# Kernel optimization log

Hardware: AMD Instinct MI355X
Metric: run time of the kernel (lower is better)

The kernel has to match this reference:

```python
import jax, jax.numpy as jnp
import numpy as np

BN_EPS = 1e-3  # keras BatchNormalization default epsilon
B, T, D, V = 2048, 100, 64, 200000
N_OTHER, V_OTHER, D_OTHER = 2, 10000, 32
DNN = (256, 128, 64)


def _gru(seq_x, Wx, Wh, b, valid, att=None):
    """GRU / AUGRU scan. seq_x [B,T,D]; valid [B,T] bool; att [B,T] or None.
    AUGRU: update gate z is scaled by the attention score a_t;
    invalid (padded) steps hold the previous state (dynamic length)."""
    Bs, Ts, _ = seq_x.shape
    H = Wh.shape[0]
    xproj = jnp.einsum('btd,dh->bth', seq_x, Wx) + b          # [B,T,3H]
    xproj = jnp.transpose(xproj, (1, 0, 2))                    # [T,B,3H]
    v = jnp.transpose(valid, (1, 0))[:, :, None]               # [T,B,1]
    if att is None:
        a = jnp.ones((Ts, Bs, 1), seq_x.dtype)
    else:
        a = jnp.transpose(att, (1, 0))[:, :, None]
    h0 = jnp.zeros((Bs, H), seq_x.dtype)

    def step(h, inp):
        xp, vi, ai = inp
        xz, xr, xh = jnp.split(xp, 3, -1)
        hz, hr, hh = jnp.split(h @ Wh, 3, -1)
        z = jax.nn.sigmoid(xz + hz) * ai
        r = jax.nn.sigmoid(xr + hr)
        cand = jnp.tanh(xh + r * hh)
        hn = (1.0 - z) * h + z * cand
        hn = jnp.where(vi, hn, h)
        return hn, hn

    final, seq = jax.lax.scan(step, h0, (xproj, v, a))
    return final, jnp.transpose(seq, (1, 0, 2))                # [B,T,H]


def _dice(x, alpha):
    # Dice activation, inference-mode BN (moving mean 0, var 1)
    p = jax.nn.sigmoid(x * (1.0 / np.sqrt(1.0 + BN_EPS)))
    return p * x + (1.0 - p) * alpha * x


def _attention(q, keys, mask, W1, b1, W2, b2, W3, b3):
    # DIN-style attention: MLP over [q, k, q-k, q*k], masked softmax over time
    qe = jnp.broadcast_to(q[:, None, :], keys.shape)
    info = jnp.concatenate([qe, keys, qe - keys, qe * keys], -1)   # [B,T,4D]
    h = jax.nn.sigmoid(info @ W1 + b1)
    h = jax.nn.sigmoid(h @ W2 + b2)
    logits = (h @ W3 + b3)[..., 0]                                  # [B,T]
    logits = jnp.where(mask, logits, jnp.float32(-1e9))
    return jax.nn.softmax(logits, axis=-1)


def setup_inputs() -> dict:
    key = jax.random.key(0)
    ks = jax.random.split(key, 32)
    s = 0.05
    inp = {
        'dense_inputs': jax.random.normal(ks[0], (B, 8), jnp.float32),
        'sparse_inputs': jax.random.randint(ks[1], (B, N_OTHER), 0, V_OTHER, jnp.int32),
        'seq_inputs': jax.random.randint(ks[2], (B, T, 1), 0, V, jnp.int32),
        'no_click_seq': jax.random.randint(ks[3], (B, T, 1), 0, V, jnp.int32),
        'item_inputs': jax.random.randint(ks[4], (B, 1), 0, V, jnp.int32),
        'hist_real_len': jax.random.randint(ks[5], (B,), 1, T + 1, jnp.int32),
        'emb_item': jax.random.normal(ks[6], (V, D), jnp.float32) * s,
        'emb_neg': jax.random.normal(ks[7], (V, D), jnp.float32) * s,
        'emb_other': jax.random.normal(ks[8], (N_OTHER, V_OTHER, D_OTHER), jnp.float32) * s,
        'gru1_Wx': jax.random.normal(ks[9], (D, 3 * D), jnp.float32) * s,
        'gru1_Wh': jax.random.normal(ks[10], (D, 3 * D), jnp.float32) * s,
        'gru1_b': jnp.zeros((3 * D,), jnp.float32),
        'att_W1': jax.random.normal(ks[11], (4 * D, 64), jnp.float32) * s,
        'att_b1': jnp.zeros((64,), jnp.float32),
        'att_W2': jax.random.normal(ks[12], (64, 16), jnp.float32) * s,
        'att_b2': jnp.zeros((16,), jnp.float32),
        'att_W3': jax.random.normal(ks[13], (16, 1), jnp.float32) * s,
        'att_b3': jnp.zeros((1,), jnp.float32),
        'gru2_Wx': jax.random.normal(ks[14], (D, 3 * D), jnp.float32) * s,
        'gru2_Wh': jax.random.normal(ks[15], (D, 3 * D), jnp.float32) * s,
        'gru2_b': jnp.zeros((3 * D,), jnp.float32),
    }
    in_dim = D + D + 8 + N_OTHER * D_OTHER  # final_state + target + other_info
    inp['bn_gamma'] = jnp.ones((in_dim,), jnp.float32)
    inp['bn_beta'] = jnp.zeros((in_dim,), jnp.float32)
    dims = (in_dim,) + DNN
    for i in range(3):
        inp[f'ffn_W{i}'] = jax.random.normal(ks[16 + i], (dims[i], dims[i + 1]), jnp.float32) * s
        inp[f'ffn_b{i}'] = jnp.zeros((dims[i + 1],), jnp.float32)
        inp[f'dice_a{i}'] = jnp.full((dims[i + 1],), 0.25, jnp.float32)
    inp['out_W'] = jax.random.normal(ks[20], (DNN[-1], 1), jnp.float32) * s
    inp['out_b'] = jnp.zeros((1,), jnp.float32)
    return inp


def reference(dense_inputs, sparse_inputs, seq_inputs, no_click_seq, item_inputs,
              hist_real_len, emb_item, emb_neg, emb_other, gru1_Wx, gru1_Wh, gru1_b,
              att_W1, att_b1, att_W2, att_b2, att_W3, att_b3, gru2_Wx, gru2_Wh, gru2_b,
              bn_gamma, bn_beta, ffn_W0, ffn_b0, dice_a0, ffn_W1, ffn_b1, dice_a1,
              ffn_W2, ffn_b2, dice_a2, out_W, out_b):
    # other (non-behavior) info: dense feats ++ other sparse embeddings
    other = jnp.concatenate(
        [dense_inputs] + [emb_other[i][sparse_inputs[:, i]] for i in range(N_OTHER)], -1)
    seq_embed = emb_item[seq_inputs[:, :, 0]]          # [B,T,D]
    neg_embed = emb_neg[no_click_seq[:, :, 0]]         # [B,T,D]
    target = emb_item[item_inputs[:, 0]]               # [B,D]
    mask = seq_inputs[:, :, 0] != 0                    # [B,T]
    valid = jnp.arange(T)[None, :] < hist_real_len[:, None]

    # interest extraction: plain GRU over behavior sequence
    _, seq_h = _gru(seq_embed, gru1_Wx, gru1_Wh, gru1_b, valid)

    # auxiliary loss: h_t should predict the next clicked item vs a negative
    m = mask[:, 1:].astype(seq_h.dtype)
    h = seq_h[:, :-1]
    p_pos = jax.nn.sigmoid(jnp.sum(h * seq_embed[:, 1:], -1))
    p_neg = jax.nn.sigmoid(jnp.sum(h * neg_embed[:, 1:], -1))
    aux_loss = -jnp.sum(m * (jnp.log(p_pos + 1e-8) + jnp.log(1.0 - p_neg + 1e-8))) / (jnp.sum(m) + 1e-8)

    # interest evolution: attention-gated AUGRU
    scores = _attention(target, seq_h, mask, att_W1, att_b1, att_W2, att_b2, att_W3, att_b3)
    final_state, _ = _gru(seq_h, gru2_Wx, gru2_Wh, gru2_b, valid, att=scores)

    x = jnp.concatenate([final_state, target, other], -1)
    x = bn_gamma * x * (1.0 / np.sqrt(1.0 + BN_EPS)) + bn_beta   # inference BN
    x = _dice(x @ ffn_W0 + ffn_b0, dice_a0)
    x = _dice(x @ ffn_W1 + ffn_b1, dice_a1)
    x = _dice(x @ ffn_W2 + ffn_b2, dice_a2)
    out = jax.nn.sigmoid(x @ out_W + out_b)                       # [B,1]
    return out, aux_loss
```

## Files before the change

kernel.cpp:

```cpp
#include <hip/hip_runtime.h>
#include <math.h>


#define DEV __device__ __forceinline__

constexpr int BB = 2048;
constexpr int TT = 100;

typedef __attribute__((ext_vector_type(8))) short bf16x8;
typedef __attribute__((ext_vector_type(4))) float f32x4;

#define MFMA16(a, b, c) __builtin_amdgcn_mfma_f32_16x16x32_bf16(a, b, c, 0, 0, 0)

DEV float sigmoidf_(float x) { return 1.0f / (1.0f + __expf(-x)); }
DEV float tanhf_(float x)    { return 1.0f - 2.0f / (__expf(2.0f * x) + 1.0f); }
DEV short f2bf(float f) {
    unsigned u = __float_as_uint(f);
    u = (u + 0x7FFFu + ((u >> 16) & 1u)) >> 16;
    return (short)u;
}
DEV float bf2f(short s) { return __uint_as_float(((unsigned)(unsigned short)s) << 16); }

__global__ void k_prep(const float* __restrict__ W1, float* Wq, float* Wk, float* Wp, float* aux_acc) {
    int i = blockIdx.x * 256 + threadIdx.x;
    if (i < 4096) {
        int k = i >> 6, c = i & 63;
        float a  = W1[k * 64 + c];
        float bb = W1[(64 + k) * 64 + c];
        float cc = W1[(128 + k) * 64 + c];
        float dd = W1[(192 + k) * 64 + c];
        Wq[i] = a + cc;
        Wk[i] = bb - cc;
        Wp[i] = dd;
    }
    if (blockIdx.x == 0 && threadIdx.x == 0) { aux_acc[0] = 0.0f; aux_acc[1] = 0.0f; }
}

__global__ __launch_bounds__(256)
void k_prepW(const float* __restrict__ Wa, const float* __restrict__ Wb,
             const float* __restrict__ Wc, const float* __restrict__ Wd,
             short* __restrict__ oa, short* __restrict__ ob,
             short* __restrict__ oc, short* __restrict__ od) {
    const float* W; short* o;
    switch (blockIdx.y) {
        case 0:  W = Wa; o = oa; break;
        case 1:  W = Wb; o = ob; break;
        case 2:  W = Wc; o = oc; break;
        default: W = Wd; o = od; break;
    }
    int d = blockIdx.x * 256 + threadIdx.x;
    int frag = d >> 9, l = (d >> 3) & 63, i = d & 7;
    int n = frag >> 1, kt = frag & 1;
    int k = kt * 32 + ((l >> 4) << 3) + i;
    int c = (n << 4) + (l & 15);
    o[d] = f2bf(W[k * 192 + c]);
}

__global__ __launch_bounds__(256)
void k_prepA(const float* __restrict__ Wk, const float* __restrict__ Wp,
             short* __restrict__ oK, short* __restrict__ oP) {
    int d = blockIdx.x * 256 + threadIdx.x;
    int mat = d >> 12, i = d & 4095;
    int f = i >> 9, l = (i >> 3) & 63, e = i & 7;
    int kt = f >> 2, n = f & 3;
    int k = kt * 32 + ((l >> 4) << 3) + e;
    int c = (n << 4) + (l & 15);
    if (mat == 0) oK[i] = f2bf(Wk[k * 64 + c]);
    else          oP[i] = f2bf(Wp[k * 64 + c]);
}

__global__ __launch_bounds__(64)
void k_target(const int* __restrict__ item, const float* __restrict__ emb_item,
              const float* __restrict__ Wq, const float* __restrict__ b1,
              float* target, float* qproj) {
    int b = blockIdx.x, c = threadIdx.x;
    __shared__ float q[64];
    int idx = item[b];
    float tv = emb_item[(size_t)idx * 64 + c];
    target[b * 64 + c] = tv;
    q[c] = tv;
    __syncthreads();
    float acc = b1[c];
#pragma unroll
    for (int k = 0; k < 64; ++k) acc = fmaf(q[k], Wq[k * 64 + c], acc);
    qproj[b * 64 + c] = acc;
}

template <int MODE>
__global__ __launch_bounds__(256, 1)
void k_scan(const int* __restrict__ seq_idx, const float* __restrict__ src,
            const short* __restrict__ WxB, const short* __restrict__ WhB,
            const float* __restrict__ bias, const int* __restrict__ hist_len,
            const float* __restrict__ scores,
            float* __restrict__ seq_out, float* __restrict__ final_out) {
    __shared__ short hA[2][1024];

    const int tid  = threadIdx.x;
    const int w    = tid >> 6;
    const int lane = tid & 63;
    const int lr   = lane & 15;
    const int kg   = lane >> 4;
    const int b0   = blockIdx.x * 8;

    for (int i = tid; i < 2048; i += 256) ((short*)hA)[i] = 0;

    bf16x8 bx[3][2], bh[3][2];
#pragma unroll
    for (int n3 = 0; n3 < 3; ++n3) {
        int n = w + n3 * 4;
#pragma unroll
        for (int kt = 0; kt < 2; ++kt) {
            bx[n3][kt] = *(const bf16x8*)(WxB + (((n * 2 + kt) * 64 + lane) << 3));
            bh[n3][kt] = *(const bf16x8*)(WhB + (((n * 2 + kt) * 64 + lane) << 3));
        }
    }

    const int   c0  = (w << 4) + lr;
    const float bz  = bias[c0];
    const float brr = bias[64 + c0];
    const float bhb = bias[128 + c0];
    const int   qc  = kg & 1;
    const bool  act = (kg < 2);

    int   hist[4];
    float h[4] = {0.f, 0.f, 0.f, 0.f};
#pragma unroll
    for (int j = 0; j < 4; ++j) hist[j] = hist_len[b0 + qc * 4 + j];

    const int rload = (lr < 8) ? lr : 7;
    float4 ec[4], en[4];
    float  scc[4] = {1.f, 1.f, 1.f, 1.f}, scn[4];

    {
        const float* eb;
        if (MODE == 0) { int idx = seq_idx[(b0 + rload) * TT]; eb = src + (size_t)idx * 64; }
        else           { eb = src + ((size_t)(b0 + rload) * TT) * 64; }
        ec[0] = *(const float4*)(eb + kg * 8);
        ec[1] = *(const float4*)(eb + kg * 8 + 4);
        ec[2] = *(const float4*)(eb + 32 + kg * 8);
        ec[3] = *(const float4*)(eb + 32 + kg * 8 + 4);
        if (MODE == 1) {
#pragma unroll
            for (int j = 0; j < 4; ++j) scc[j] = scores[(b0 + qc * 4 + j) * TT];
        }
    }
    __syncthreads();

    for (int t = 0; t < TT; ++t) {
        const int buf = t & 1;
        const int so0 = lr * 64 + (((kg    ) ^ (lr & 7)) << 3);
        const int so1 = lr * 64 + (((4 + kg) ^ (lr & 7)) << 3);
        bf16x8 ha0 = *(const bf16x8*)&hA[buf][so0];
        bf16x8 ha1 = *(const bf16x8*)&hA[buf][so1];

        if (t < TT - 1) {
            const float* eb;
            if (MODE == 0) { int idx = seq_idx[(b0 + rload) * TT + t + 1]; eb = src + (size_t)idx * 64; }
            else           { eb = src + ((size_t)(b0 + rload) * TT + (t + 1)) * 64; }
            en[0] = *(const float4*)(eb + kg * 8);
            en[1] = *(const float4*)(eb + kg * 8 + 4);
            en[2] = *(const float4*)(eb + 32 + kg * 8);
            en[3] = *(const float4*)(eb + 32 + kg * 8 + 4);
            if (MODE == 1) {
#pragma unroll
                for (int j = 0; j < 4; ++j) scn[j] = scores[(b0 + qc * 4 + j) * TT + t + 1];
            }
        }

        bf16x8 ea0, ea1;
        ea0[0] = f2bf(ec[0].x); ea0[1] = f2bf(ec[0].y); ea0[2] = f2bf(ec[0].z); ea0[3] = f2bf(ec[0].w);
        ea0[4] = f2bf(ec[1].x); ea0[5] = f2bf(ec[1].y); ea0[6] = f2bf(ec[1].z); ea0[7] = f2bf(ec[1].w);
        ea1[0] = f2bf(ec[2].x); ea1[1] = f2bf(ec[2].y); ea1[2] = f2bf(ec[2].z); ea1[3] = f2bf(ec[2].w);
        ea1[4] = f2bf(ec[3].x); ea1[5] = f2bf(ec[3].y); ea1[6] = f2bf(ec[3].z); ea1[7] = f2bf(ec[3].w);

        f32x4 az  = {0.f, 0.f, 0.f, 0.f};
        f32x4 ar  = {0.f, 0.f, 0.f, 0.f};
        f32x4 ahx = {0.f, 0.f, 0.f, 0.f};
        f32x4 ahh = {0.f, 0.f, 0.f, 0.f};
        az  = MFMA16(ea0, bx[0][0], az);  az  = MFMA16(ea1, bx[0][1], az);
        az  = MFMA16(ha0, bh[0][0], az);  az  = MFMA16(ha1, bh[0][1], az);
        ar  = MFMA16(ea0, bx[1][0], ar);  ar  = MFMA16(ea1, bx[1][1], ar);
        ar  = MFMA16(ha0, bh[1][0], ar);  ar  = MFMA16(ha1, bh[1][1], ar);
        ahx = MFMA16(ea0, bx[2][0], ahx); ahx = MFMA16(ea1, bx[2][1], ahx);
        ahh = MFMA16(ha0, bh[2][0], ahh); ahh = MFMA16(ha1, bh[2][1], ahh);

        if (act) {
#pragma unroll
            for (int j = 0; j < 4; ++j) {
                float a01  = (MODE == 1) ? scc[j] : 1.0f;
                float z    = sigmoidf_(az[j] + bz) * a01;
                float r    = sigmoidf_(ar[j] + brr);
                float cand = tanhf_(ahx[j] + bhb + r * ahh[j]);
                float hn   = h[j] + z * (cand - h[j]);
                h[j] = (t < hist[j]) ? hn : h[j];
                int rr = qc * 4 + j;
                int sw = rr * 64 + ((((c0 >> 3)) ^ (rr & 7)) << 3) + (c0 & 7);
                hA[buf ^ 1][sw] = f2bf(h[j]);
                if (MODE == 0)
                    seq_out[((size_t)(b0 + rr) * TT + t) * 64 + c0] = h[j];
            }
        }
        if (t < TT - 1) {
#pragma unroll
            for (int q4 = 0; q4 < 4; ++q4) ec[q4] = en[q4];
            if (MODE == 1) {
#pragma unroll
                for (int j = 0; j < 4; ++j) scc[j] = scn[j];
            }
        }
        __syncthreads();
    }

    if (MODE == 1 && act) {
#pragma unroll
        for (int j = 0; j < 4; ++j) {
            int rr = qc * 4 + j;
            final_out[(b0 + rr) * 64 + c0] = h[j];
        }
    }
}

__global__ __launch_bounds__(256)
void k_attn(const float* __restrict__ seq_h, const float* __restrict__ target,
            const float* __restrict__ qproj, const int* __restrict__ seq_idx,
            const short* __restrict__ WkB, const short* __restrict__ WpB,
            const float* __restrict__ W2g, const float* __restrict__ b2g,
            const float* __restrict__ W3g, const float* __restrict__ b3g,
            float* __restrict__ scores) {
    __shared__ __align__(16) short keysb[7168];
    __shared__ __align__(16) short pkb[7168];
    __shared__ float W2_s[1024];
    __shared__ float q_s[64], qp_s[64];
    __shared__ float b2_s[16], W3_s[16];
    __shared__ float lg[112];

    const int b = blockIdx.x, tid = threadIdx.x;
    const int w = tid >> 6, lane = tid & 63;

    bf16x8 BK[2][4], BP[2][4];
#pragma unroll
    for (int kt = 0; kt < 2; ++kt)
#pragma unroll
        for (int n = 0; n < 4; ++n) {
            BK[kt][n] = *(const bf16x8*)(WkB + (((kt * 4 + n) * 64 + lane) << 3));
            BP[kt][n] = *(const bf16x8*)(WpB + (((kt * 4 + n) * 64 + lane) << 3));
        }
    if (tid < 64)  { q_s[tid] = target[b * 64 + tid]; qp_s[tid] = qproj[b * 64 + tid]; }
    if (tid >= 64 && tid < 80) { b2_s[tid - 64] = b2g[tid - 64]; W3_s[tid - 64] = W3g[tid - 64]; }
    for (int i = tid; i < 1024; i += 256) W2_s[i] = W2g[i];
    __syncthreads();

    for (int i4 = tid; i4 < 1792; i4 += 256) {
        int r = i4 >> 4, c4 = i4 & 15;
        short4 kv, pv;
        if (r < TT) {
            float4 f = *(const float4*)(seq_h + (size_t)b * (TT * 64) + r * 64 + c4 * 4);
            float q0 = q_s[c4 * 4], q1 = q_s[c4 * 4 + 1], q2 = q_s[c4 * 4 + 2], q3 = q_s[c4 * 4 + 3];
            kv = make_short4(f2bf(f.x), f2bf(f.y), f2bf(f.z), f2bf(f.w));
            pv = make_short4(f2bf(f.x * q0), f2bf(f.y * q1), f2bf(f.z * q2), f2bf(f.w * q3));
        } else {
            kv = make_short4(0, 0, 0, 0); pv = kv;
        }
        int off = r * 128 + ((c4 * 8) ^ ((r & 7) << 4));
        *(short4*)((char*)keysb + off) = kv;
        *(short4*)((char*)pkb + off)   = pv;
    }
    __syncthreads();

    for (int rt = w; rt < 7; rt += 4) {
        const int r0 = rt * 16;
        const int arow = r0 + (lane & 15);
        const int kb = lane >> 4;
        bf16x8 AK[2], AP[2];
#pragma unroll
        for (int kt = 0; kt < 2; ++kt) {
            int off = arow * 128 + (((kt * 64) + kb * 16) ^ ((arow & 7) << 4));
            AK[kt] = *(const bf16x8*)((const char*)keysb + off);
            AP[kt] = *(const bf16x8*)((const char*)pkb + off);
        }
        f32x4 C[4];
#pragma unroll
        for (int n = 0; n < 4; ++n) { C[n] = (f32x4){0.f, 0.f, 0.f, 0.f}; }
#pragma unroll
        for (int n = 0; n < 4; ++n) {
            C[n] = MFMA16(AK[0], BK[0][n], C[n]);
            C[n] = MFMA16(AK[1], BK[1][n], C[n]);
            C[n] = MFMA16(AP[0], BP[0][n], C[n]);
            C[n] = MFMA16(AP[1], BP[1][n], C[n]);
        }
#pragma unroll
        for (int n = 0; n < 4; ++n) {
            int col = n * 16 + (lane & 15);
            float qp = qp_s[col];
#pragma unroll
            for (int j = 0; j < 4; ++j) {
                int row = r0 + (lane >> 4) * 4 + j;
                float h1 = sigmoidf_(C[n][j] + qp);
                int off = row * 128 + ((col * 2) ^ ((row & 7) << 4));
                *(short*)((char*)pkb + off) = f2bf(h1);
            }
        }
    }
    __syncthreads();

    {
        int t = tid >> 1, half = tid & 1;
        if (t < TT) {
            int j0 = half * 8;
            float acc[8];
#pragma unroll
            for (int jj = 0; jj < 8; ++jj) acc[jj] = b2_s[j0 + jj];
#pragma unroll
            for (int ch = 0; ch < 8; ++ch) {
                int off = t * 128 + ((ch * 16) ^ ((t & 7) << 4));
                bf16x8 hv = *(const bf16x8*)((const char*)pkb + off);
#pragma unroll
                for (int e = 0; e < 8; ++e) {
                    float hf = bf2f(hv[e]);
                    int k = ch * 8 + e;
#pragma unroll
                    for (int jj = 0; jj < 8; ++jj)
                        acc[jj] = fmaf(hf, W2_s[k * 16 + j0 + jj], acc[jj]);
                }
            }
            float part = 0.f;
#pragma unroll
            for (int jj = 0; jj < 8; ++jj) part += sigmoidf_(acc[jj]) * W3_s[j0 + jj];
            part += __shfl_xor(part, 1);
            if (half == 0) {
                bool m = (seq_idx[b * TT + t] != 0);
                lg[t] = m ? (part + b3g[0]) : -1e9f;
            }
        }
    }
    __syncthreads();

    if (w == 0) {
        float a  = lg[lane];
        float bv = (lane + 64 < TT) ? lg[lane + 64] : -1e30f;
        float mx = fmaxf(a, bv);
#pragma unroll
        for (int s = 32; s; s >>= 1) mx = fmaxf(mx, __shfl_xor(mx, s));
        float ea = __expf(a - mx);
        float eb = (lane + 64 < TT) ? __expf(bv - mx) : 0.f;
        float sum = ea + eb;
#pragma unroll
        for (int s = 32; s; s >>= 1) sum += __shfl_xor(sum, s);
        float inv = 1.0f / sum;
        scores[b * TT + lane] = ea * inv;
        if (lane + 64 < TT) scores[b * TT + lane + 64] = eb * inv;
    }
}

__global__ __launch_bounds__(64)
void k_aux(const float* __restrict__ seq_h, const int* __restrict__ seq_idx,
           const int* __restrict__ neg_idx, const float* __restrict__ emb_item,
           const float* __restrict__ emb_neg, float* aux_acc) {
    int b = blockIdx.x, l = threadIdx.x;
    float num = 0.0f;
    float den = 0.0f;
    for (int t = 0; t < TT - 1; ++t) {
        int ip = seq_idx[b * TT + t + 1];
        int in_ = neg_idx[b * TT + t + 1];
        float h = seq_h[(size_t)b * (TT * 64) + t * 64 + l];
        float dp = h * emb_item[(size_t)ip * 64 + l];
        float dn = h * emb_neg[(size_t)in_ * 64 + l];
#pragma unroll
        for (int s = 32; s; s >>= 1) { dp += __shfl_xor(dp, s); dn += __shfl_xor(dn, s); }
        if (l == 0 && ip != 0) {
            float pp = sigmoidf_(dp), pn = sigmoidf_(dn);
            num += __logf(pp + 1e-8f) + __logf(1.0f - pn + 1e-8f);
            den += 1.0f;
        }
    }
    if (l == 0) {
        atomicAdd(&aux_acc[0], num);
        atomicAdd(&aux_acc[1], den);
    }
}

__global__ __launch_bounds__(256)
void k_mlp(const float* __restrict__ final_state, const float* __restrict__ target,
           const float* __restrict__ dense, const int* __restrict__ sparse,
           const float* __restrict__ emb_other,
           const float* __restrict__ bng, const float* __restrict__ bnb,
           const float* __restrict__ W0, const float* __restrict__ bb0, const float* __restrict__ al0,
           const float* __restrict__ W1, const float* __restrict__ bb1, const float* __restrict__ al1,
           const float* __restrict__ W2, const float* __restrict__ bb2, const float* __restrict__ al2,
           const float* __restrict__ Wo, const float* __restrict__ bo,
           const float* __restrict__ aux_acc, float* __restrict__ out) {
    const float inv1 = 0.9995003747f;
    int tid = threadIdx.x, b0 = blockIdx.x * 8;
    __shared__ float x_s[8][200], h1_s[8][256], h2_s[8][128], h3_s[8][64];

    for (int i = tid; i < 8 * 200; i += 256) {
        int r = i / 200, cc = i - r * 200, b = b0 + r;
        float v;
        if (cc < 64)       v = final_state[b * 64 + cc];
        else if (cc < 128) v = target[b * 64 + cc - 64];
        else if (cc < 136) v = dense[b * 8 + cc - 128];
        else if (cc < 168) v = emb_other[(size_t)sparse[b * 2 + 0] * 32 + (cc - 136)];
        else               v = emb_other[(size_t)10000 * 32 + (size_t)sparse[b * 2 + 1] * 32 + (cc - 168)];
        x_s[r][cc] = fmaf(bng[cc] * inv1, v, bnb[cc]);
    }
    __syncthreads();
    {
        int r = tid >> 5, cb = tid & 31;
        float acc[8];
#pragma unroll
        for (int j = 0; j < 8; ++j) acc[j] = bb0[cb + 32 * j];
        for (int k = 0; k < 200; ++k) {
            float xv = x_s[r][k];
#pragma unroll
            for (int j = 0; j < 8; ++j) acc[j] = fmaf(xv, W0[k * 256 + cb + 32 * j], acc[j]);
        }
#pragma unroll
        for (int j = 0; j < 8; ++j) {
            float y = acc[j];
            float p = sigmoidf_(y * inv1);
            h1_s[r][cb + 32 * j] = y * (p + (1.0f - p) * al0[cb + 32 * j]);
        }
    }
    __syncthreads();
    {
        int r = tid >> 5, cb = tid & 31;
        float acc[4];
#pragma unroll
        for (int j = 0; j < 4; ++j) acc[j] = bb1[cb + 32 * j];
        for (int k = 0; k < 256; ++k) {
            float xv = h1_s[r][k];
#pragma unroll
            for (int j = 0; j < 4; ++j) acc[j] = fmaf(xv, W1[k * 128 + cb + 32 * j], acc[j]);
        }
#pragma unroll
        for (int j = 0; j < 4; ++j) {
            float y = acc[j];
            float p = sigmoidf_(y * inv1);
            h2_s[r][cb + 32 * j] = y * (p + (1.0f - p) * al1[cb + 32 * j]);
        }
    }
    __syncthreads();
    {
        int r = tid >> 5, cb = tid & 31;
        float acc[2] = {bb2[cb], bb2[cb + 32]};
        for (int k = 0; k < 128; ++k) {
            float xv = h2_s[r][k];
            acc[0] = fmaf(xv, W2[k * 64 + cb], acc[0]);
            acc[1] = fmaf(xv, W2[k * 64 + cb + 32], acc[1]);
        }
#pragma unroll
        for (int j = 0; j < 2; ++j) {
            float y = acc[j];
            float p = sigmoidf_(y * inv1);
            h3_s[r][cb + 32 * j] = y * (p + (1.0f - p) * al2[cb + 32 * j]);
        }
    }
    __syncthreads();
    {
        int r = tid >> 5, l = tid & 31;
        float v = h3_s[r][l] * Wo[l] + h3_s[r][l + 32] * Wo[l + 32];
#pragma unroll
        for (int s = 16; s; s >>= 1) v += __shfl_xor(v, s, 32);
        if (l == 0) out[b0 + r] = sigmoidf_(v + bo[0]);
    }
    if (blockIdx.x == 0 && tid == 0) {
        out[BB] = -aux_acc[0] / (aux_acc[1] + 1e-8f);
    }
}

extern "C" void kernel_launch(void* const* d_in, const int* in_sizes, int n_in,
                              void* d_out, int out_size, void* d_ws, size_t ws_size,
                              hipStream_t stream) {
    (void)in_sizes; (void)n_in; (void)out_size; (void)ws_size;
    const float* dense    = (const float*)d_in[0];
    const int*   sparse   = (const int*)d_in[1];
    const int*   seq_in   = (const int*)d_in[2];
    const int*   neg_in   = (const int*)d_in[3];
    const int*   item_in  = (const int*)d_in[4];
    const int*   hist     = (const int*)d_in[5];
    const float* emb_item = (const float*)d_in[6];
    const float* emb_neg  = (const float*)d_in[7];
    const float* emb_oth  = (const float*)d_in[8];
    const float* g1Wx = (const float*)d_in[9];
    const float* g1Wh = (const float*)d_in[10];
    const float* g1b  = (const float*)d_in[11];
    const float* aW1  = (const float*)d_in[12];
    const float* ab1  = (const float*)d_in[13];
    const float* aW2  = (const float*)d_in[14];
    const float* ab2  = (const float*)d_in[15];
    const float* aW3  = (const float*)d_in[16];
    const float* ab3  = (const float*)d_in[17];
    const float* g2Wx = (const float*)d_in[18];
    const float* g2Wh = (const float*)d_in[19];
    const float* g2b  = (const float*)d_in[20];
    const float* bng  = (const float*)d_in[21];
    const float* bnb  = (const float*)d_in[22];
    const float* W0   = (const float*)d_in[23];
    const float* b0f  = (const float*)d_in[24];
    const float* a0f  = (const float*)d_in[25];
    const float* W1f  = (const float*)d_in[26];
    const float* b1f  = (const float*)d_in[27];
    const float* a1f  = (const float*)d_in[28];
    const float* W2f  = (const float*)d_in[29];
    const float* b2f  = (const float*)d_in[30];
    const float* a2f  = (const float*)d_in[31];
    const float* Wo   = (const float*)d_in[32];
    const float* bo   = (const float*)d_in[33];

    float* ws          = (float*)d_ws;
    float* seq_h       = ws;
    float* scoresW     = seq_h + 13107200;
    float* target      = scoresW + 204800;
    float* qproj       = target + 131072;
    float* final_state = qproj + 131072;
    float* Wq          = final_state + 131072;
    float* Wk          = Wq + 4096;
    float* Wp          = Wk + 4096;
    short* WxB1        = (short*)(Wp + 4096);
    short* WhB1        = WxB1 + 12288;
    short* WxB2        = WhB1 + 12288;
    short* WhB2        = WxB2 + 12288;
    short* WkB         = WhB2 + 12288;
    short* WpB         = WkB + 4096;
    float* aux_acc     = (float*)(WpB + 4096);

    k_prep<<<16, 256, 0, stream>>>(aW1, Wq, Wk, Wp, aux_acc);
    k_prepW<<<dim3(48, 4), 256, 0, stream>>>(g1Wx, g1Wh, g2Wx, g2Wh, WxB1, WhB1, WxB2, WhB2);
    k_prepA<<<32, 256, 0, stream>>>(Wk, Wp, WkB, WpB);
    k_target<<<BB, 64, 0, stream>>>(item_in, emb_item, Wq, ab1, target, qproj);
    k_scan<0><<<256, 256, 0, stream>>>(seq_in, emb_item, WxB1, WhB1, g1b, hist, nullptr, seq_h, nullptr);
    k_attn<<<BB, 256, 0, stream>>>(seq_h, target, qproj, seq_in, WkB, WpB, aW2, ab2, aW3, ab3, scoresW);
    k_scan<1><<<256, 256, 0, stream>>>(seq_in, seq_h, WxB2, WhB2, g2b, hist, scoresW, nullptr, final_state);
    k_aux<<<BB, 64, 0, stream>>>(seq_h, seq_in, neg_in, emb_item, emb_neg, aux_acc);
    k_mlp<<<256, 256, 0, stream>>>(final_state, target, dense, sparse, emb_oth, bng, bnb,
                                   W0, b0f, a0f, W1f, b1f, a1f, W2f, b2f, a2f, Wo, bo,
                                   aux_acc, (float*)d_out);
}
```

Baseline: 598.4 us.

## Store GRU hidden sequence as bf16 and halve per-block batch rows in scans

The first GRU's hidden-state sequence is now written as bf16 instead of fp32, halving its memory traffic for the attention, second-scan and aux kernels, which read it directly. Each scan block now handles 4 batch rows instead of 8, doubling the grid to 512 blocks with 2 blocks per CU for more parallelism on the latency-bound recurrence. The per-step block barrier is replaced by a lightweight LDS-only wait plus s_barrier, and the bf16 conversion of the next embedding is deferred until after the gate math. The aux kernel is spread over 4 waves per batch row. The cost is a lower-precision stored hidden state (the aux loss sees bf16 h) and half of each MFMA tile's rows doing wasted work.

```diff
diff --git a/kernel.cpp b/kernel.cpp
--- a/kernel.cpp
+++ b/kernel.cpp
@@ -20,6 +20,12 @@
     return (short)u;
 }
 DEV float bf2f(short s) { return __uint_as_float(((unsigned)(unsigned short)s) << 16); }
+
+DEV void sync_lds() {
+    __builtin_amdgcn_sched_barrier(0);
+    asm volatile("s_waitcnt lgkmcnt(0)\n\ts_barrier" ::: "memory");
+    __builtin_amdgcn_sched_barrier(0);
+}
 
 __global__ void k_prep(const float* __restrict__ W1, float* Wq, float* Wk, float* Wp, float* aux_acc) {
     int i = blockIdx.x * 256 + threadIdx.x;
@@ -87,12 +93,13 @@
 }
 
 template <int MODE>
-__global__ __launch_bounds__(256, 1)
-void k_scan(const int* __restrict__ seq_idx, const float* __restrict__ src,
+__global__ __launch_bounds__(256, 2)
+void k_scan(const int* __restrict__ seq_idx, const float* __restrict__ embf,
+            const short* __restrict__ seqb,
             const short* __restrict__ WxB, const short* __restrict__ WhB,
             const float* __restrict__ bias, const int* __restrict__ hist_len,
             const float* __restrict__ scores,
-            float* __restrict__ seq_out, float* __restrict__ final_out) {
+            short* __restrict__ seq_out, float* __restrict__ final_out) {
     __shared__ short hA[2][1024];
 
     const int tid  = threadIdx.x;
@@ -100,7 +107,7 @@
     const int lane = tid & 63;
     const int lr   = lane & 15;
     const int kg   = lane >> 4;
-    const int b0   = blockIdx.x * 8;
+    const int b0   = blockIdx.x * 4;
 
     for (int i = tid; i < 2048; i += 256) ((short*)hA)[i] = 0;
 
@@ -119,70 +126,80 @@
     const float bz  = bias[c0];
     const float brr = bias[64 + c0];
     const float bhb = bias[128 + c0];
-    const int   qc  = kg & 1;
-    const bool  act = (kg < 2);
+    const bool  act = (kg == 0);
 
     int   hist[4];
     float h[4] = {0.f, 0.f, 0.f, 0.f};
 #pragma unroll
-    for (int j = 0; j < 4; ++j) hist[j] = hist_len[b0 + qc * 4 + j];
-
-    const int rload = (lr < 8) ? lr : 7;
-    float4 ec[4], en[4];
-    float  scc[4] = {1.f, 1.f, 1.f, 1.f}, scn[4];
+    for (int j = 0; j < 4; ++j) hist[j] = hist_len[b0 + j];
+
+    const int rload = (lr < 4) ? lr : 3;
+    bf16x8 ecb0, ecb1;
+    float  scc[4] = {1.f, 1.f, 1.f, 1.f};
 
     {
-        const float* eb;
-        if (MODE == 0) { int idx = seq_idx[(b0 + rload) * TT]; eb = src + (size_t)idx * 64; }
-        else           { eb = src + ((size_t)(b0 + rload) * TT) * 64; }
-        ec[0] = *(const float4*)(eb + kg * 8);
-        ec[1] = *(const float4*)(eb + kg * 8 + 4);
-        ec[2] = *(const float4*)(eb + 32 + kg * 8);
-        ec[3] = *(const float4*)(eb + 32 + kg * 8 + 4);
+        if (MODE == 0) {
+            int idx = seq_idx[(b0 + rload) * TT];
+            const float* eb = embf + (size_t)idx * 64;
+            float4 f0 = *(const float4*)(eb + kg * 8);
+            float4 f1 = *(const float4*)(eb + kg * 8 + 4);
+            float4 f2 = *(const float4*)(eb + 32 + kg * 8);
+            float4 f3 = *(const float4*)(eb + 32 + kg * 8 + 4);
+            ecb0[0] = f2bf(f0.x); ecb0[1] = f2bf(f0.y); ecb0[2] = f2bf(f0.z); ecb0[3] = f2bf(f0.w);
+            ecb0[4] = f2bf(f1.x); ecb0[5] = f2bf(f1.y); ecb0[6] = f2bf(f1.z); ecb0[7] = f2bf(f1.w);
+            ecb1[0] = f2bf(f2.x); ecb1[1] = f2bf(f2.y); ecb1[2] = f2bf(f2.z); ecb1[3] = f2bf(f2.w);
+            ecb1[4] = f2bf(f3.x); ecb1[5] = f2bf(f3.y); ecb1[6] = f2bf(f3.z); ecb1[7] = f2bf(f3.w);
+        } else {
+            const short* eb = seqb + ((size_t)(b0 + rload) * TT) * 64;
+            ecb0 = *(const bf16x8*)(eb + kg * 8);
+            ecb1 = *(const bf16x8*)(eb + 32 + kg * 8);
+        }
         if (MODE == 1) {
 #pragma unroll
-            for (int j = 0; j < 4; ++j) scc[j] = scores[(b0 + qc * 4 + j) * TT];
-        }
-    }
-    __syncthreads();
+            for (int j = 0; j < 4; ++j) scc[j] = scores[(b0 + j) * TT];
+        }
+    }
+    __syncthreads();
+
+    const int so0 = lr * 64 + (((kg    ) ^ (lr & 7)) << 3);
+    const int so1 = lr * 64 + (((4 + kg) ^ (lr & 7)) << 3);
 
     for (int t = 0; t < TT; ++t) {
         const int buf = t & 1;
-        const int so0 = lr * 64 + (((kg    ) ^ (lr & 7)) << 3);
-        const int so1 = lr * 64 + (((4 + kg) ^ (lr & 7)) << 3);
         bf16x8 ha0 = *(const bf16x8*)&hA[buf][so0];
         bf16x8 ha1 = *(const bf16x8*)&hA[buf][so1];
 
-        if (t < TT - 1) {
-            const float* eb;
-            if (MODE == 0) { int idx = seq_idx[(b0 + rload) * TT + t + 1]; eb = src + (size_t)idx * 64; }
-            else           { eb = src + ((size_t)(b0 + rload) * TT + (t + 1)) * 64; }
-            en[0] = *(const float4*)(eb + kg * 8);
-            en[1] = *(const float4*)(eb + kg * 8 + 4);
-            en[2] = *(const float4*)(eb + 32 + kg * 8);
-            en[3] = *(const float4*)(eb + 32 + kg * 8 + 4);
-            if (MODE == 1) {
-#pragma unroll
-                for (int j = 0; j < 4; ++j) scn[j] = scores[(b0 + qc * 4 + j) * TT + t + 1];
+        float4 f0, f1, f2, f3;
+        bf16x8 nb0, nb1;
+        float scn[4];
+        const bool haven = (t < TT - 1);
+        if (haven) {
+            if (MODE == 0) {
+                int idx = seq_idx[(b0 + rload) * TT + t + 1];
+                const float* eb = embf + (size_t)idx * 64;
+                f0 = *(const float4*)(eb + kg * 8);
+                f1 = *(const float4*)(eb + kg * 8 + 4);
+                f2 = *(const float4*)(eb + 32 + kg * 8);
+                f3 = *(const float4*)(eb + 32 + kg * 8 + 4);
+            } else {
+                const short* eb = seqb + ((size_t)(b0 + rload) * TT + (t + 1)) * 64;
+                nb0 = *(const bf16x8*)(eb + kg * 8);
+                nb1 = *(const bf16x8*)(eb + 32 + kg * 8);
+#pragma unroll
+                for (int j = 0; j < 4; ++j) scn[j] = scores[(b0 + j) * TT + t + 1];
             }
         }
-
-        bf16x8 ea0, ea1;
-        ea0[0] = f2bf(ec[0].x); ea0[1] = f2bf(ec[0].y); ea0[2] = f2bf(ec[0].z); ea0[3] = f2bf(ec[0].w);
-        ea0[4] = f2bf(ec[1].x); ea0[5] = f2bf(ec[1].y); ea0[6] = f2bf(ec[1].z); ea0[7] = f2bf(ec[1].w);
-        ea1[0] = f2bf(ec[2].x); ea1[1] = f2bf(ec[2].y); ea1[2] = f2bf(ec[2].z); ea1[3] = f2bf(ec[2].w);
-        ea1[4] = f2bf(ec[3].x); ea1[5] = f2bf(ec[3].y); ea1[6] = f2bf(ec[3].z); ea1[7] = f2bf(ec[3].w);
 
         f32x4 az  = {0.f, 0.f, 0.f, 0.f};
         f32x4 ar  = {0.f, 0.f, 0.f, 0.f};
         f32x4 ahx = {0.f, 0.f, 0.f, 0.f};
         f32x4 ahh = {0.f, 0.f, 0.f, 0.f};
-        az  = MFMA16(ea0, bx[0][0], az);  az  = MFMA16(ea1, bx[0][1], az);
-        az  = MFMA16(ha0, bh[0][0], az);  az  = MFMA16(ha1, bh[0][1], az);
-        ar  = MFMA16(ea0, bx[1][0], ar);  ar  = MFMA16(ea1, bx[1][1], ar);
-        ar  = MFMA16(ha0, bh[1][0], ar);  ar  = MFMA16(ha1, bh[1][1], ar);
-        ahx = MFMA16(ea0, bx[2][0], ahx); ahx = MFMA16(ea1, bx[2][1], ahx);
-        ahh = MFMA16(ha0, bh[2][0], ahh); ahh = MFMA16(ha1, bh[2][1], ahh);
+        az  = MFMA16(ecb0, bx[0][0], az);  az  = MFMA16(ecb1, bx[0][1], az);
+        az  = MFMA16(ha0,  bh[0][0], az);  az  = MFMA16(ha1,  bh[0][1], az);
+        ar  = MFMA16(ecb0, bx[1][0], ar);  ar  = MFMA16(ecb1, bx[1][1], ar);
+        ar  = MFMA16(ha0,  bh[1][0], ar);  ar  = MFMA16(ha1,  bh[1][1], ar);
+        ahx = MFMA16(ecb0, bx[2][0], ahx); ahx = MFMA16(ecb1, bx[2][1], ahx);
+        ahh = MFMA16(ha0,  bh[2][0], ahh); ahh = MFMA16(ha1,  bh[2][1], ahh);
 
         if (act) {
 #pragma unroll
@@ -193,35 +210,38 @@
                 float cand = tanhf_(ahx[j] + bhb + r * ahh[j]);
                 float hn   = h[j] + z * (cand - h[j]);
                 h[j] = (t < hist[j]) ? hn : h[j];
-                int rr = qc * 4 + j;
-                int sw = rr * 64 + ((((c0 >> 3)) ^ (rr & 7)) << 3) + (c0 & 7);
-                hA[buf ^ 1][sw] = f2bf(h[j]);
+                short v = f2bf(h[j]);
+                int sw = j * 64 + (((c0 >> 3) ^ j) << 3) + (c0 & 7);
+                hA[buf ^ 1][sw] = v;
                 if (MODE == 0)
-                    seq_out[((size_t)(b0 + rr) * TT + t) * 64 + c0] = h[j];
+                    seq_out[((size_t)(b0 + j) * TT + t) * 64 + c0] = v;
             }
         }
-        if (t < TT - 1) {
-#pragma unroll
-            for (int q4 = 0; q4 < 4; ++q4) ec[q4] = en[q4];
-            if (MODE == 1) {
+
+        if (haven) {
+            if (MODE == 0) {
+                ecb0[0] = f2bf(f0.x); ecb0[1] = f2bf(f0.y); ecb0[2] = f2bf(f0.z); ecb0[3] = f2bf(f0.w);
+                ecb0[4] = f2bf(f1.x); ecb0[5] = f2bf(f1.y); ecb0[6] = f2bf(f1.z); ecb0[7] = f2bf(f1.w);
+                ecb1[0] = f2bf(f2.x); ecb1[1] = f2bf(f2.y); ecb1[2] = f2bf(f2.z); ecb1[3] = f2bf(f2.w);
+                ecb1[4] = f2bf(f3.x); ecb1[5] = f2bf(f3.y); ecb1[6] = f2bf(f3.z); ecb1[7] = f2bf(f3.w);
+            } else {
+                ecb0 = nb0; ecb1 = nb1;
 #pragma unroll
                 for (int j = 0; j < 4; ++j) scc[j] = scn[j];
             }
         }
-        __syncthreads();
+        sync_lds();
     }
 
     if (MODE == 1 && act) {
 #pragma unroll
-        for (int j = 0; j < 4; ++j) {
-            int rr = qc * 4 + j;
-            final_out[(b0 + rr) * 64 + c0] = h[j];
-        }
+        for (int j = 0; j < 4; ++j)
+            final_out[(b0 + j) * 64 + c0] = h[j];
     }
 }
 
 __global__ __launch_bounds__(256)
-void k_attn(const float* __restrict__ seq_h, const float* __restrict__ target,
+void k_attn(const short* __restrict__ seq_h, const float* __restrict__ target,
             const float* __restrict__ qproj, const int* __restrict__ seq_idx,
             const short* __restrict__ WkB, const short* __restrict__ WpB,
             const float* __restrict__ W2g, const float* __restrict__ b2g,
@@ -254,10 +274,11 @@
         int r = i4 >> 4, c4 = i4 & 15;
         short4 kv, pv;
         if (r < TT) {
-            float4 f = *(const float4*)(seq_h + (size_t)b * (TT * 64) + r * 64 + c4 * 4);
+            short4 sv = *(const short4*)(seq_h + (size_t)b * (TT * 64) + r * 64 + c4 * 4);
             float q0 = q_s[c4 * 4], q1 = q_s[c4 * 4 + 1], q2 = q_s[c4 * 4 + 2], q3 = q_s[c4 * 4 + 3];
-            kv = make_short4(f2bf(f.x), f2bf(f.y), f2bf(f.z), f2bf(f.w));
-            pv = make_short4(f2bf(f.x * q0), f2bf(f.y * q1), f2bf(f.z * q2), f2bf(f.w * q3));
+            kv = sv;
+            pv = make_short4(f2bf(bf2f(sv.x) * q0), f2bf(bf2f(sv.y) * q1),
+                             f2bf(bf2f(sv.z) * q2), f2bf(bf2f(sv.w) * q3));
         } else {
             kv = make_short4(0, 0, 0, 0); pv = kv;
         }
@@ -352,17 +373,20 @@
     }
 }
 
-__global__ __launch_bounds__(64)
-void k_aux(const float* __restrict__ seq_h, const int* __restrict__ seq_idx,
+__global__ __launch_bounds__(256)
+void k_aux(const short* __restrict__ seq_h, const int* __restrict__ seq_idx,
            const int* __restrict__ neg_idx, const float* __restrict__ emb_item,
            const float* __restrict__ emb_neg, float* aux_acc) {
-    int b = blockIdx.x, l = threadIdx.x;
-    float num = 0.0f;
-    float den = 0.0f;
-    for (int t = 0; t < TT - 1; ++t) {
-        int ip = seq_idx[b * TT + t + 1];
+    int b = blockIdx.x, tid = threadIdx.x;
+    int w = tid >> 6, l = tid & 63;
+    __shared__ float pnum[4], pden[4];
+    float num = 0.0f, den = 0.0f;
+    for (int i = 0; i < 25; ++i) {
+        int t = w + i * 4;
+        if (t >= TT - 1) break;
+        int ip  = seq_idx[b * TT + t + 1];
         int in_ = neg_idx[b * TT + t + 1];
-        float h = seq_h[(size_t)b * (TT * 64) + t * 64 + l];
+        float h = bf2f(seq_h[(size_t)b * (TT * 64) + t * 64 + l]);
         float dp = h * emb_item[(size_t)ip * 64 + l];
         float dn = h * emb_neg[(size_t)in_ * 64 + l];
 #pragma unroll
@@ -373,9 +397,11 @@
             den += 1.0f;
         }
     }
-    if (l == 0) {
-        atomicAdd(&aux_acc[0], num);
-        atomicAdd(&aux_acc[1], den);
+    if (l == 0) { pnum[w] = num; pden[w] = den; }
+    __syncthreads();
+    if (tid == 0) {
+        atomicAdd(&aux_acc[0], pnum[0] + pnum[1] + pnum[2] + pnum[3]);
+        atomicAdd(&aux_acc[1], pden[0] + pden[1] + pden[2] + pden[3]);
     }
 }
 
@@ -508,8 +534,8 @@
     const float* bo   = (const float*)d_in[33];
 
     float* ws          = (float*)d_ws;
-    float* seq_h       = ws;
-    float* scoresW     = seq_h + 13107200;
+    short* seq_hb      = (short*)ws;
+    float* scoresW     = ws + 6553600;
     float* target      = scoresW + 204800;
     float* qproj       = target + 131072;
     float* final_state = qproj + 131072;
@@ -528,10 +554,12 @@
     k_prepW<<<dim3(48, 4), 256, 0, stream>>>(g1Wx, g1Wh, g2Wx, g2Wh, WxB1, WhB1, WxB2, WhB2);
     k_prepA<<<32, 256, 0, stream>>>(Wk, Wp, WkB, WpB);
     k_target<<<BB, 64, 0, stream>>>(item_in, emb_item, Wq, ab1, target, qproj);
-    k_scan<0><<<256, 256, 0, stream>>>(seq_in, emb_item, WxB1, WhB1, g1b, hist, nullptr, seq_h, nullptr);
-    k_attn<<<BB, 256, 0, stream>>>(seq_h, target, qproj, seq_in, WkB, WpB, aW2, ab2, aW3, ab3, scoresW);
-    k_scan<1><<<256, 256, 0, stream>>>(seq_in, seq_h, WxB2, WhB2, g2b, hist, scoresW, nullptr, final_state);
-    k_aux<<<BB, 64, 0, stream>>>(seq_h, seq_in, neg_in, emb_item, emb_neg, aux_acc);
+    k_scan<0><<<512, 256, 0, stream>>>(seq_in, emb_item, nullptr, WxB1, WhB1, g1b, hist,
+                                       nullptr, seq_hb, nullptr);
+    k_attn<<<BB, 256, 0, stream>>>(seq_hb, target, qproj, seq_in, WkB, WpB, aW2, ab2, aW3, ab3, scoresW);
+    k_scan<1><<<512, 256, 0, stream>>>(seq_in, nullptr, seq_hb, WxB2, WhB2, g2b, hist,
+                                       scoresW, nullptr, final_state);
+    k_aux<<<BB, 256, 0, stream>>>(seq_hb, seq_in, neg_in, emb_item, emb_neg, aux_acc);
     k_mlp<<<256, 256, 0, stream>>>(final_state, target, dense, sparse, emb_oth, bng, bnb,
                                    W0, b0f, a0f, W1f, b1f, a1f, W2f, b2f, a2f, Wo, bo,
                                    aux_acc, (float*)d_out);
```

New measurement: 598.2 us. Within noise of the previous version (-0.0%).
